# Kernel tuning notes

Hardware: AMD Instinct MI355X
Metric: run time of the kernel (lower is better)

The kernel has to match this reference:

```python
import jax, jax.numpy as jnp
import numpy as np

B, Q, K, F = 4, 512, 512, 32
DV = 32          # vnode feature dim
H = 64           # proj_vs output dim
FM = 2 * F + DV + 2 + 1 + 1 + 1  # = 101, pairwise concat feature dim
H1, H2 = 256, 64 # proj_scores hidden widths
MAX_DIST = 1e30  # default max_dist = inf


def _dense_init(key, fan_in, fan_out):
    kw, kb = jax.random.split(key)
    W = jax.random.normal(kw, (fan_in, fan_out), jnp.float32) / np.sqrt(fan_in)
    b = jnp.zeros((fan_out,), jnp.float32)
    return W, b


def setup_inputs() -> dict:
    key = jax.random.key(0)
    ks_ = jax.random.split(key, 13)
    qs = jax.random.normal(ks_[0], (B, Q, F), jnp.float32)
    ks = jax.random.normal(ks_[1], (B, K, F), jnp.float32)
    vs = jax.random.normal(ks_[2], (B, K, F), jnp.float32)
    vnode = jax.random.normal(ks_[3], (B, 1, DV), jnp.float32)
    qs_s = jax.random.normal(ks_[4], (B, Q, 2), jnp.float32)
    ks_s = jax.random.normal(ks_[5], (B, K, 2), jnp.float32)
    qs_t = jnp.ones((B, Q, 1), jnp.float32)                     # queries at t=1
    ks_t = jax.random.uniform(ks_[6], (B, K, 1), jnp.float32)   # keys in [0,1)
    valid_lens = jax.random.randint(ks_[7], (B,), 1, K + 1).astype(jnp.int32)
    Ws1, bs1 = _dense_init(ks_[8], FM, H1)
    Ws2, bs2 = _dense_init(ks_[9], H1, H2)
    Ws3, bs3 = _dense_init(ks_[10], H2, 1)
    Wv, bv = _dense_init(ks_[11], F, H)
    return {"qs": qs, "ks": ks, "vs": vs, "vnode": vnode,
            "qs_s": qs_s, "ks_s": ks_s, "qs_t": qs_t, "ks_t": ks_t,
            "Ws1": Ws1, "bs1": bs1, "Ws2": Ws2, "bs2": bs2,
            "Ws3": Ws3, "bs3": bs3, "Wv": Wv, "bv": bv,
            "valid_lens": valid_lens}


def reference(qs, ks, vs, vnode, qs_s, ks_s, qs_t, ks_t,
              Ws1, bs1, Ws2, bs2, Ws3, bs3, Wv, bv, valid_lens):
    Bq, Qq, Ff = qs.shape
    Kk = ks.shape[1]
    # pairwise broadcast of q/k/vnode features -> [B, Q, K, *]
    qe = jnp.broadcast_to(qs[:, :, None, :], (Bq, Qq, Kk, Ff))
    ke = jnp.broadcast_to(ks[:, None, :, :], (Bq, Qq, Kk, Ff))
    vn = jnp.broadcast_to(vnode[:, :, None, :], (Bq, Qq, Kk, vnode.shape[-1]))
    # spatial pairwise features
    s_diff = qs_s[:, :, None, :] - ks_s[:, None, :, :]          # [B,Q,K,2]
    s_dist = jnp.linalg.norm(s_diff, axis=-1, keepdims=True)    # [B,Q,K,1]
    s_dist_sq = jnp.square(s_dist)
    # temporal pairwise feature
    t_diff = qs_t[:, :, None, :] - ks_t[:, None, :, :]          # [B,Q,K,1]
    m = jnp.concatenate([qe, ke, vn, s_diff, s_dist, s_dist_sq, t_diff], axis=-1)
    # mask: valid key length, spatial radius, causal time
    key_mask = jnp.arange(Kk)[None, :] < valid_lens[:, None]    # [B,K]
    mask = key_mask[:, None, :]                                  # [B,1,K] -> broadcast [B,Q,K]
    mask = jnp.logical_and(mask, s_dist[..., 0] <= MAX_DIST)
    mask = jnp.logical_and(mask, t_diff[..., 0] >= 0)
    # proj_scores MLP: Dense-gelu-Dense-gelu-Dense
    h = jax.nn.gelu(m @ Ws1 + bs1)
    h = jax.nn.gelu(h @ Ws2 + bs2)
    scores = (h @ Ws3 + bs3)[..., 0]                             # [B,Q,K]
    scores = jnp.where(mask, scores, -jnp.inf)
    attn = jax.nn.softmax(scores, axis=-1)
    vproj = vs @ Wv + bv                                         # [B,K,H]
    ctx = jnp.einsum('bqk,bkh->bqh', attn, vproj)
    return ctx, attn
```

## Files before the change

### kernel.cpp

```cpp
#include <hip/hip_runtime.h>

#define B_ 4
#define Q_ 512
#define K_ 512
#define F_ 32
#define H1_ 256
#define H2_ 64
#define HV_ 64

typedef unsigned short u16;
typedef unsigned int u32;

typedef float f32x4 __attribute__((ext_vector_type(4)));
typedef short short8 __attribute__((ext_vector_type(8)));
typedef __bf16 bfv8 __attribute__((ext_vector_type(8)));
union FRG { short8 s; bfv8 h; u32 u[4]; };

#define OFF_QS   0
#define OFF_KS   65536
#define OFF_VS   131072
#define OFF_VN   196608
#define OFF_QSS  196736
#define OFF_KSS  200832
#define OFF_QST  204928
#define OFF_KST  206976
#define OFF_W1   209024
#define OFF_B1   234880
#define OFF_W2   235136
#define OFF_B2   243328
#define OFF_W3   243392
#define OFF_B3   243456
#define OFF_WV   243460
#define OFF_BV   245508
#define OFF_VL   245572
#define OFF_AQ   262144
#define OFF_AK   786432
#define OFF_VP   1310720

__device__ __forceinline__ float bf2f(u16 u) {
    union { u32 u; float f; } c; c.u = ((u32)u) << 16; return c.f;
}
__device__ __forceinline__ u16 f2bf(float f) {
    union { float f; u32 u; } c; c.f = f;
    u32 u = c.u;
    return (u16)((u + 0x7FFFu + ((u >> 16) & 1u)) >> 16);
}
__device__ __forceinline__ float gelu_t(float x) {
    const float Kb = 2.3022082f;
    const float Kc = 0.10294324f;
    float y = x * __builtin_fmaf(Kc, x * x, Kb);
    float e = __builtin_amdgcn_exp2f(y);
    return x - x * __builtin_amdgcn_rcpf(e + 1.0f);
}

__global__ __launch_bounds__(256) void convert_kernel(
    const void* s0, const void* s1, const void* s2, const void* s3,
    const void* s4, const void* s5, const void* s6, const void* s7,
    const void* s8, const void* s9, const void* s10, const void* s11,
    const void* s12, const void* s13, const void* s14, const void* s15,
    const void* s16, float* wsf)
{
    int blk = blockIdx.x, t = threadIdx.x;
    int bf16m = (((const u32*)s6)[0] != 0x3F800000u);

    if (blk == 963) {
        if (t < 4) {
            const int* vi = (const int*)s16;
            int is64 = (vi[1] == 0);
            ((int*)(wsf + OFF_VL))[t] = vi[is64 ? 2 * t : t];
        }
        return;
    }
    if (blk >= 919 && blk < 951) {
        int idx = (blk - 919) * 256 + t;
        int r  = idx & 3;
        int l  = (idx >> 2) & 63;
        int n  = (idx >> 8) & 3;
        int ks = idx >> 10;
        int k0  = ks * 32 + (l >> 4) * 8 + 2 * r;
        int col = n * 16 + (l & 15);
        u16 lo, hi;
        if (bf16m) {
            lo = ((const u16*)s10)[k0 * H2_ + col];
            hi = ((const u16*)s10)[(k0 + 1) * H2_ + col];
        } else {
            lo = f2bf(((const float*)s10)[k0 * H2_ + col]);
            hi = f2bf(((const float*)s10)[(k0 + 1) * H2_ + col]);
        }
        ((u32*)(wsf + OFF_W2))[idx] = (u32)lo | ((u32)hi << 16);
        return;
    }
    const void* src; int n, dst, b0;
    if      (blk < 256) { src = s0;  n = 65536; dst = OFF_QS;  b0 = 0;   }
    else if (blk < 512) { src = s1;  n = 65536; dst = OFF_KS;  b0 = 256; }
    else if (blk < 768) { src = s2;  n = 65536; dst = OFF_VS;  b0 = 512; }
    else if (blk < 769) { src = s3;  n = 128;   dst = OFF_VN;  b0 = 768; }
    else if (blk < 785) { src = s4;  n = 4096;  dst = OFF_QSS; b0 = 769; }
    else if (blk < 801) { src = s5;  n = 4096;  dst = OFF_KSS; b0 = 785; }
    else if (blk < 809) { src = s6;  n = 2048;  dst = OFF_QST; b0 = 801; }
    else if (blk < 817) { src = s7;  n = 2048;  dst = OFF_KST; b0 = 809; }
    else if (blk < 918) { src = s8;  n = 25856; dst = OFF_W1;  b0 = 817; }
    else if (blk < 919) { src = s9;  n = 256;   dst = OFF_B1;  b0 = 918; }
    else if (blk < 952) { src = s11; n = 64;    dst = OFF_B2;  b0 = 951; }
    else if (blk < 953) { src = s12; n = 64;    dst = OFF_W3;  b0 = 952; }
    else if (blk < 954) { src = s13; n = 1;     dst = OFF_B3;  b0 = 953; }
    else if (blk < 962) { src = s14; n = 2048;  dst = OFF_WV;  b0 = 954; }
    else                { src = s15; n = 64;    dst = OFF_BV;  b0 = 962; }
    int idx = (blk - b0) * 256 + t;
    if (idx < n)
        (wsf + dst)[idx] = bf16m ? bf2f(((const u16*)src)[idx]) : ((const float*)src)[idx];
}

__global__ __launch_bounds__(256) void prep_kernel(
    const float* __restrict__ qs, const float* __restrict__ ks, const float* __restrict__ vs,
    const float* __restrict__ vnode, const float* __restrict__ qs_s, const float* __restrict__ ks_s,
    const float* __restrict__ qs_t, const float* __restrict__ ks_t,
    const float* __restrict__ W1, const float* __restrict__ b1,
    const float* __restrict__ Wv, const float* __restrict__ bv,
    float* __restrict__ Aq, float* __restrict__ Ak, float* __restrict__ vproj)
{
    int blk = blockIdx.x;
    int t = threadIdx.x;
    if (blk < 2048) {
        int b = blk >> 9, q = blk & 511, d = t;
        float acc = b1[d];
        const float* qrow = qs + (b * Q_ + q) * F_;
        #pragma unroll
        for (int f = 0; f < F_; ++f)
            acc = __builtin_fmaf(qrow[f], W1[f * H1_ + d], acc);
        const float* vn = vnode + b * 32;
        #pragma unroll
        for (int f = 0; f < 32; ++f)
            acc = __builtin_fmaf(vn[f], W1[(64 + f) * H1_ + d], acc);
        float q0 = qs_s[(b * Q_ + q) * 2 + 0];
        float q1 = qs_s[(b * Q_ + q) * 2 + 1];
        float qt = qs_t[b * Q_ + q];
        acc = __builtin_fmaf(q0, W1[96 * H1_ + d], acc);
        acc = __builtin_fmaf(q1, W1[97 * H1_ + d], acc);
        acc = __builtin_fmaf(qt, W1[100 * H1_ + d], acc);
        Aq[blk * H1_ + d] = acc;
    } else if (blk < 4096) {
        int rk = blk - 2048;
        int b = rk >> 9, k = rk & 511, d = t;
        float acc = 0.f;
        const float* krow = ks + (b * K_ + k) * F_;
        #pragma unroll
        for (int f = 0; f < F_; ++f)
            acc = __builtin_fmaf(krow[f], W1[(32 + f) * H1_ + d], acc);
        float k0 = ks_s[(b * K_ + k) * 2 + 0];
        float k1 = ks_s[(b * K_ + k) * 2 + 1];
        float kt = ks_t[b * K_ + k];
        acc = __builtin_fmaf(-k0, W1[96 * H1_ + d], acc);
        acc = __builtin_fmaf(-k1, W1[97 * H1_ + d], acc);
        acc = __builtin_fmaf(-kt, W1[100 * H1_ + d], acc);
        Ak[(b * K_ + k) * H1_ + d] = acc;
    } else {
        int idx = (blk - 4096) * 256 + t;
        int h = idx & 63;
        int k = (idx >> 6) & 511;
        int b = idx >> 15;
        float acc = bv[h];
        const float* vrow = vs + (b * K_ + k) * F_;
        #pragma unroll
        for (int f = 0; f < F_; ++f)
            acc = __builtin_fmaf(vrow[f], Wv[f * HV_ + h], acc);
        vproj[idx] = acc;
    }
}

__global__ __launch_bounds__(512, 4) void fused_kernel(
    const float* __restrict__ qs_s, const float* __restrict__ ks_s,
    const float* __restrict__ qs_t, const float* __restrict__ ks_t,
    const float* __restrict__ W1, const u32* __restrict__ W2F,
    const float* __restrict__ b2, const float* __restrict__ W3, const float* __restrict__ b3,
    const int* __restrict__ vl, const float* __restrict__ Aq, const float* __restrict__ Ak,
    const float* __restrict__ vproj, const void* __restrict__ qs_t_src, void* __restrict__ d_out)
{
    __shared__ __align__(16) float sAq[2][H1_];
    __shared__ __align__(16) float sw98[H1_], sw99[H1_];
    __shared__ float sScore[2][K_];
    __shared__ float sE[2][K_];
    __shared__ float sRed[2][12];
    __shared__ float sPart[2][8][HV_];

    int q0 = blockIdx.x * 2, b = blockIdx.y, t = threadIdx.x;
    int lane = t & 63, w = t >> 6;
    int VL = vl[b];
    int nT = (VL + 15) >> 4;

    if (t < H1_) {
        sAq[0][t] = Aq[(b * Q_ + q0) * H1_ + t];
        sAq[1][t] = Aq[(b * Q_ + q0 + 1) * H1_ + t];
        sw98[t] = W1[98 * H1_ + t];
        sw99[t] = W1[99 * H1_ + t];
    }
    __syncthreads();

    float qx0[2], qx1[2], qtv[2];
    #pragma unroll
    for (int qq = 0; qq < 2; ++qq) {
        qx0[qq] = qs_s[(b * Q_ + q0 + qq) * 2 + 0];
        qx1[qq] = qs_s[(b * Q_ + q0 + qq) * 2 + 1];
        qtv[qq] = qs_t[b * Q_ + q0 + qq];
    }

    float b2c[4], w3c[4];
    #pragma unroll
    for (int n = 0; n < 4; ++n) {
        int col = n * 16 + (lane & 15);
        b2c[n] = b2[col];
        w3c[n] = W3[col];
    }
    float b3v = b3[0];
    const float* Ak_b = Ak + (size_t)b * K_ * H1_;
    int lgrp = (lane >> 4) * 8;

    for (int tile = w; tile < nT; tile += 8) {
        int row = tile * 16 + (lane & 15);
        float c0 = ks_s[(b * K_ + row) * 2 + 0];
        float c1 = ks_s[(b * K_ + row) * 2 + 1];
        float ktv = ks_t[b * K_ + row];
        float dsq[2], dist[2], okf[2];
        #pragma unroll
        for (int qq = 0; qq < 2; ++qq) {
            float d0 = qx0[qq] - c0, d1 = qx1[qq] - c1;
            dsq[qq]  = __builtin_fmaf(d0, d0, d1 * d1);
            dist[qq] = sqrtf(dsq[qq]);
            okf[qq] = (row < VL && (qtv[qq] - ktv) >= 0.f && dist[qq] <= 1e30f) ? 1.f : 0.f;
        }

        f32x4 acc[2][4];
        #pragma unroll
        for (int qq = 0; qq < 2; ++qq)
            #pragma unroll
            for (int n = 0; n < 4; ++n) acc[qq][n] = (f32x4){0.f, 0.f, 0.f, 0.f};

        const float* akrow = Ak_b + row * H1_;
        #pragma unroll 2
        for (int ks = 0; ks < 8; ++ks) {
            int dbase = ks * 32 + lgrp;
            f32x4 w98a = *(const f32x4*)&sw98[dbase];
            f32x4 w98b = *(const f32x4*)&sw98[dbase + 4];
            f32x4 w99a = *(const f32x4*)&sw99[dbase];
            f32x4 w99b = *(const f32x4*)&sw99[dbase + 4];
            f32x4 ak0 = *(const f32x4*)(akrow + dbase);
            f32x4 ak1 = *(const f32x4*)(akrow + dbase + 4);
            short8 bf[4];
            #pragma unroll
            for (int n = 0; n < 4; ++n)
                bf[n] = *(const short8*)&W2F[((ks * 4 + n) * 64 + lane) * 4];
            FRG fa[2];
            #pragma unroll
            for (int qq = 0; qq < 2; ++qq) {
                f32x4 aqa = *(const f32x4*)&sAq[qq][dbase];
                f32x4 aqb = *(const f32x4*)&sAq[qq][dbase + 4];
                #pragma unroll
                for (int j = 0; j < 4; ++j) {
                    float pre = ak0[j] + __builtin_fmaf(dist[qq], w98a[j],
                               __builtin_fmaf(dsq[qq], w99a[j], aqa[j]));
                    fa[qq].h[j] = (__bf16)gelu_t(pre);
                }
                #pragma unroll
                for (int j = 0; j < 4; ++j) {
                    float pre = ak1[j] + __builtin_fmaf(dist[qq], w98b[j],
                               __builtin_fmaf(dsq[qq], w99b[j], aqb[j]));
                    fa[qq].h[4 + j] = (__bf16)gelu_t(pre);
                }
            }
            #pragma unroll
            for (int n = 0; n < 4; ++n) {
                acc[0][n] = __builtin_amdgcn_mfma_f32_16x16x32_bf16(fa[0].s, bf[n], acc[0][n], 0, 0, 0);
                acc[1][n] = __builtin_amdgcn_mfma_f32_16x16x32_bf16(fa[1].s, bf[n], acc[1][n], 0, 0, 0);
            }
        }

        #pragma unroll
        for (int qq = 0; qq < 2; ++qq) {
            float s0 = 0.f, s1 = 0.f, s2 = 0.f, s3 = 0.f;
            #pragma unroll
            for (int n = 0; n < 4; ++n) {
                f32x4 a = acc[qq][n];
                s0 = __builtin_fmaf(gelu_t(a.x + b2c[n]), w3c[n], s0);
                s1 = __builtin_fmaf(gelu_t(a.y + b2c[n]), w3c[n], s1);
                s2 = __builtin_fmaf(gelu_t(a.z + b2c[n]), w3c[n], s2);
                s3 = __builtin_fmaf(gelu_t(a.w + b2c[n]), w3c[n], s3);
            }
            #pragma unroll
            for (int off = 1; off < 16; off <<= 1) {
                s0 += __shfl_xor(s0, off);
                s1 += __shfl_xor(s1, off);
                s2 += __shfl_xor(s2, off);
                s3 += __shfl_xor(s3, off);
            }
            int g = lane >> 4;
            float ok0 = __shfl(okf[qq], g * 4 + 0);
            float ok1 = __shfl(okf[qq], g * 4 + 1);
            float ok2 = __shfl(okf[qq], g * 4 + 2);
            float ok3 = __shfl(okf[qq], g * 4 + 3);
            if ((lane & 15) == 0) {
                int r0 = tile * 16 + g * 4;
                const float NEG = -__builtin_inff();
                sScore[qq][r0 + 0] = (ok0 != 0.f) ? s0 + b3v : NEG;
                sScore[qq][r0 + 1] = (ok1 != 0.f) ? s1 + b3v : NEG;
                sScore[qq][r0 + 2] = (ok2 != 0.f) ? s2 + b3v : NEG;
                sScore[qq][r0 + 3] = (ok3 != 0.f) ? s3 + b3v : NEG;
            }
        }
    }
    __syncthreads();

    const float NEG = -__builtin_inff();
    float v[2], mr[2];
    #pragma unroll
    for (int qq = 0; qq < 2; ++qq) {
        v[qq] = (t < VL) ? sScore[qq][t] : NEG;
        mr[qq] = v[qq];
    }
    #pragma unroll
    for (int off = 32; off > 0; off >>= 1) {
        mr[0] = fmaxf(mr[0], __shfl_down(mr[0], off));
        mr[1] = fmaxf(mr[1], __shfl_down(mr[1], off));
    }
    if (lane == 0) { sRed[0][w] = mr[0]; sRed[1][w] = mr[1]; }
    __syncthreads();
    if (t == 0) {
        float m0 = sRed[0][0], m1 = sRed[1][0];
        #pragma unroll
        for (int i = 1; i < 8; ++i) {
            m0 = fmaxf(m0, sRed[0][i]);
            m1 = fmaxf(m1, sRed[1][i]);
        }
        sRed[0][8] = m0; sRed[1][8] = m1;
    }
    __syncthreads();

    const float L2E = 1.4426950408889634f;
    float e[2], sum[2];
    #pragma unroll
    for (int qq = 0; qq < 2; ++qq) {
        float mx = sRed[qq][8];
        int fin = (mx > -1e37f);
        e[qq] = (fin && v[qq] > -1e37f) ? __builtin_amdgcn_exp2f((v[qq] - mx) * L2E) : 0.f;
        sE[qq][t] = e[qq];
        sum[qq] = e[qq];
    }
    #pragma unroll
    for (int off = 32; off > 0; off >>= 1) {
        sum[0] += __shfl_down(sum[0], off);
        sum[1] += __shfl_down(sum[1], off);
    }
    if (lane == 0) { sRed[0][w] = sum[0]; sRed[1][w] = sum[1]; }
    __syncthreads();
    if (t == 0) {
        float s0 = 0.f, s1 = 0.f;
        #pragma unroll
        for (int i = 0; i < 8; ++i) { s0 += sRed[0][i]; s1 += sRed[1][i]; }
        sRed[0][8] = (s0 > 0.f) ? 1.f / s0 : 0.f;
        sRed[1][8] = (s1 > 0.f) ? 1.f / s1 : 0.f;
    }
    __syncthreads();
    float rinv[2] = { sRed[0][8], sRed[1][8] };

    int bf16m = (((const u32*)qs_t_src)[0] != 0x3F800000u);
    #pragma unroll
    for (int qq = 0; qq < 2; ++qq) {
        int oattn = B_ * Q_ * HV_ + (b * Q_ + q0 + qq) * K_ + t;
        if (bf16m) ((u16*)d_out)[oattn] = f2bf(e[qq] * rinv[qq]);
        else       ((float*)d_out)[oattn] = e[qq] * rinv[qq];
    }

    int h = t & 63, ksp = t >> 6;
    const float* vp = vproj + b * K_ * HV_ + h;
    float a0 = 0.f, a1 = 0.f;
    int kbeg = ksp * 64;
    for (int kk = kbeg; kk < kbeg + 64; ++kk) {
        float vv = vp[kk * HV_];
        a0 = __builtin_fmaf(sE[0][kk], vv, a0);
        a1 = __builtin_fmaf(sE[1][kk], vv, a1);
    }
    sPart[0][ksp][h] = a0;
    sPart[1][ksp][h] = a1;
    __syncthreads();
    if (t < 128) {
        int qq = t >> 6, hh = t & 63;
        float c = 0.f;
        #pragma unroll
        for (int p = 0; p < 8; ++p) c += sPart[qq][p][hh];
        c *= rinv[qq];
        int octx = (b * Q_ + q0 + qq) * HV_ + hh;
        if (bf16m) ((u16*)d_out)[octx] = f2bf(c);
        else       ((float*)d_out)[octx] = c;
    }
}

extern "C" void kernel_launch(void* const* d_in, const int* in_sizes, int n_in,
                              void* d_out, int out_size, void* d_ws, size_t ws_size,
                              hipStream_t stream) {
    float* wsf = (float*)d_ws;

    convert_kernel<<<dim3(964), dim3(256), 0, stream>>>(
        d_in[0], d_in[1], d_in[2], d_in[3], d_in[4], d_in[5], d_in[6], d_in[7],
        d_in[8], d_in[9], d_in[10], d_in[11], d_in[12], d_in[13], d_in[14], d_in[15],
        d_in[16], wsf);

    prep_kernel<<<dim3(4608), dim3(256), 0, stream>>>(
        wsf + OFF_QS, wsf + OFF_KS, wsf + OFF_VS, wsf + OFF_VN,
        wsf + OFF_QSS, wsf + OFF_KSS, wsf + OFF_QST, wsf + OFF_KST,
        wsf + OFF_W1, wsf + OFF_B1, wsf + OFF_WV, wsf + OFF_BV,
        wsf + OFF_AQ, wsf + OFF_AK, wsf + OFF_VP);

    fused_kernel<<<dim3(Q_ / 2, B_), dim3(512), 0, stream>>>(
        wsf + OFF_QSS, wsf + OFF_KSS, wsf + OFF_QST, wsf + OFF_KST,
        wsf + OFF_W1, (const u32*)(wsf + OFF_W2), wsf + OFF_B2, wsf + OFF_W3, wsf + OFF_B3,
        (const int*)(wsf + OFF_VL), wsf + OFF_AQ, wsf + OFF_AK, wsf + OFF_VP,
        d_in[6], d_out);
}
```

Measured before the change: 84.29 us.

## Switch MLP layer-2 MFMA to fp16 with packed conversion, DPP reductions, interleaved batch grid

Stores the second-layer weights and the gelu activations as fp16, using the packed round-toward-zero convert instead of a per-element bf16 cast, and issues fp16 MFMA instead of bf16. The 16-lane score reduction now uses DPP row shifts instead of shuffles, so the final value is written from lane 15. The grid is flattened with batch as the fastest index, which spreads blocks from batches with different valid lengths evenly across the device. The goal is fewer conversion and shuffle instructions in the hot loop and better load balance, at the cost of fp16's narrower range.

```diff
diff --git a/kernel.cpp b/kernel.cpp
--- a/kernel.cpp
+++ b/kernel.cpp
@@ -12,9 +12,10 @@
 typedef unsigned int u32;
 
 typedef float f32x4 __attribute__((ext_vector_type(4)));
-typedef short short8 __attribute__((ext_vector_type(8)));
-typedef __bf16 bfv8 __attribute__((ext_vector_type(8)));
-union FRG { short8 s; bfv8 h; u32 u[4]; };
+typedef _Float16 h8 __attribute__((ext_vector_type(8)));
+typedef __fp16 fp16x2 __attribute__((ext_vector_type(2)));
+union FRG16 { h8 v; u32 u[4]; };
+union H2U { fp16x2 p; u32 u; };
 
 #define OFF_QS   0
 #define OFF_KS   65536
@@ -52,6 +53,15 @@
     float e = __builtin_amdgcn_exp2f(y);
     return x - x * __builtin_amdgcn_rcpf(e + 1.0f);
 }
+__device__ __forceinline__ float row16_sum(float x) {
+    union { float f; int i; } c, o;
+    c.f = x;
+    o.i = __builtin_amdgcn_update_dpp(0, c.i, 0x111, 0xF, 0xF, true); c.f += o.f;
+    o.i = __builtin_amdgcn_update_dpp(0, c.i, 0x112, 0xF, 0xF, true); c.f += o.f;
+    o.i = __builtin_amdgcn_update_dpp(0, c.i, 0x114, 0xF, 0xF, true); c.f += o.f;
+    o.i = __builtin_amdgcn_update_dpp(0, c.i, 0x118, 0xF, 0xF, true); c.f += o.f;
+    return c.f;
+}
 
 __global__ __launch_bounds__(256) void convert_kernel(
     const void* s0, const void* s1, const void* s2, const void* s3,
@@ -79,15 +89,16 @@
         int ks = idx >> 10;
         int k0  = ks * 32 + (l >> 4) * 8 + 2 * r;
         int col = n * 16 + (l & 15);
-        u16 lo, hi;
+        float flo, fhi;
         if (bf16m) {
-            lo = ((const u16*)s10)[k0 * H2_ + col];
-            hi = ((const u16*)s10)[(k0 + 1) * H2_ + col];
+            flo = bf2f(((const u16*)s10)[k0 * H2_ + col]);
+            fhi = bf2f(((const u16*)s10)[(k0 + 1) * H2_ + col]);
         } else {
-            lo = f2bf(((const float*)s10)[k0 * H2_ + col]);
-            hi = f2bf(((const float*)s10)[(k0 + 1) * H2_ + col]);
-        }
-        ((u32*)(wsf + OFF_W2))[idx] = (u32)lo | ((u32)hi << 16);
+            flo = ((const float*)s10)[k0 * H2_ + col];
+            fhi = ((const float*)s10)[(k0 + 1) * H2_ + col];
+        }
+        H2U pk; pk.p = __builtin_amdgcn_cvt_pkrtz(flo, fhi);
+        ((u32*)(wsf + OFF_W2))[idx] = pk.u;
         return;
     }
     const void* src; int n, dst, b0;
@@ -183,7 +194,10 @@
     __shared__ float sRed[2][12];
     __shared__ float sPart[2][8][HV_];
 
-    int q0 = blockIdx.x * 2, b = blockIdx.y, t = threadIdx.x;
+    int bid = blockIdx.x;
+    int b = bid & 3;
+    int q0 = (bid >> 2) * 2;
+    int t = threadIdx.x;
     int lane = t & 63, w = t >> 6;
     int VL = vl[b];
     int nT = (VL + 15) >> 4;
@@ -245,32 +259,38 @@
             f32x4 w99b = *(const f32x4*)&sw99[dbase + 4];
             f32x4 ak0 = *(const f32x4*)(akrow + dbase);
             f32x4 ak1 = *(const f32x4*)(akrow + dbase + 4);
-            short8 bf[4];
+            FRG16 fb[4];
             #pragma unroll
             for (int n = 0; n < 4; ++n)
-                bf[n] = *(const short8*)&W2F[((ks * 4 + n) * 64 + lane) * 4];
-            FRG fa[2];
+                fb[n].v = *(const h8*)&W2F[((ks * 4 + n) * 64 + lane) * 4];
+            FRG16 fa[2];
             #pragma unroll
             for (int qq = 0; qq < 2; ++qq) {
                 f32x4 aqa = *(const f32x4*)&sAq[qq][dbase];
                 f32x4 aqb = *(const f32x4*)&sAq[qq][dbase + 4];
+                float g[8];
                 #pragma unroll
                 for (int j = 0; j < 4; ++j) {
                     float pre = ak0[j] + __builtin_fmaf(dist[qq], w98a[j],
                                __builtin_fmaf(dsq[qq], w99a[j], aqa[j]));
-                    fa[qq].h[j] = (__bf16)gelu_t(pre);
+                    g[j] = gelu_t(pre);
                 }
                 #pragma unroll
                 for (int j = 0; j < 4; ++j) {
                     float pre = ak1[j] + __builtin_fmaf(dist[qq], w98b[j],
                                __builtin_fmaf(dsq[qq], w99b[j], aqb[j]));
-                    fa[qq].h[4 + j] = (__bf16)gelu_t(pre);
+                    g[4 + j] = gelu_t(pre);
+                }
+                #pragma unroll
+                for (int j = 0; j < 4; ++j) {
+                    H2U pk; pk.p = __builtin_amdgcn_cvt_pkrtz(g[2 * j], g[2 * j + 1]);
+                    fa[qq].u[j] = pk.u;
                 }
             }
             #pragma unroll
             for (int n = 0; n < 4; ++n) {
-                acc[0][n] = __builtin_amdgcn_mfma_f32_16x16x32_bf16(fa[0].s, bf[n], acc[0][n], 0, 0, 0);
-                acc[1][n] = __builtin_amdgcn_mfma_f32_16x16x32_bf16(fa[1].s, bf[n], acc[1][n], 0, 0, 0);
+                acc[0][n] = __builtin_amdgcn_mfma_f32_16x16x32_f16(fa[0].v, fb[n].v, acc[0][n], 0, 0, 0);
+                acc[1][n] = __builtin_amdgcn_mfma_f32_16x16x32_f16(fa[1].v, fb[n].v, acc[1][n], 0, 0, 0);
             }
         }
 
@@ -285,19 +305,16 @@
                 s2 = __builtin_fmaf(gelu_t(a.z + b2c[n]), w3c[n], s2);
                 s3 = __builtin_fmaf(gelu_t(a.w + b2c[n]), w3c[n], s3);
             }
-            #pragma unroll
-            for (int off = 1; off < 16; off <<= 1) {
-                s0 += __shfl_xor(s0, off);
-                s1 += __shfl_xor(s1, off);
-                s2 += __shfl_xor(s2, off);
-                s3 += __shfl_xor(s3, off);
-            }
+            s0 = row16_sum(s0);
+            s1 = row16_sum(s1);
+            s2 = row16_sum(s2);
+            s3 = row16_sum(s3);
             int g = lane >> 4;
             float ok0 = __shfl(okf[qq], g * 4 + 0);
             float ok1 = __shfl(okf[qq], g * 4 + 1);
             float ok2 = __shfl(okf[qq], g * 4 + 2);
             float ok3 = __shfl(okf[qq], g * 4 + 3);
-            if ((lane & 15) == 0) {
+            if ((lane & 15) == 15) {
                 int r0 = tile * 16 + g * 4;
                 const float NEG = -__builtin_inff();
                 sScore[qq][r0 + 0] = (ok0 != 0.f) ? s0 + b3v : NEG;
@@ -409,7 +426,7 @@
         wsf + OFF_W1, wsf + OFF_B1, wsf + OFF_WV, wsf + OFF_BV,
         wsf + OFF_AQ, wsf + OFF_AK, wsf + OFF_VP);
 
-    fused_kernel<<<dim3(Q_ / 2, B_), dim3(512), 0, stream>>>(
+    fused_kernel<<<dim3(Q_ / 2 * B_), dim3(512), 0, stream>>>(
         wsf + OFF_QSS, wsf + OFF_KSS, wsf + OFF_QST, wsf + OFF_KST,
         wsf + OFF_W1, (const u32*)(wsf + OFF_W2), wsf + OFF_B2, wsf + OFF_W3, wsf + OFF_B3,
         (const int*)(wsf + OFF_VL), wsf + OFF_AQ, wsf + OFF_AK, wsf + OFF_VP,
```

After: 143.1 us. 69.8% more time.
